# Kernel tuning notes

Measured on AMD Instinct MI355X. Metric: run time of the kernel, lower is better.

Reference implementation:

```python
import jax, jax.numpy as jnp
import numpy as np

SP_D, SP_H = 22, 11   # att_dim, number of vertical strips
EPS = 1e-5
ITER_N = 5            # Newton-Schulz iterations


def setup_inputs() -> dict:
    key = jax.random.key(0)
    ks = jax.random.split(key, 16)
    B, C, H, W = 64, 1024, 44, 16
    f = jnp.float32
    return {
        'x': jax.random.normal(ks[0], (B, C, H, W), dtype=f),
        'dr_w': jax.random.normal(ks[1], (SP_D, C), dtype=f) * 0.02,
        'dr_b': jax.random.normal(ks[2], (SP_D,), dtype=f) * 0.01,
        'bn1_g': 1.0 + 0.1 * jax.random.normal(ks[3], (SP_D,), dtype=f),
        'bn1_b': 0.1 * jax.random.normal(ks[4], (SP_D,), dtype=f),
        'bn1_m': 0.1 * jax.random.normal(ks[5], (SP_D,), dtype=f),
        'bn1_v': jax.random.uniform(ks[6], (SP_D,), dtype=f, minval=0.5, maxval=1.5),
        'rbn_g': 1.0 + 0.1 * jax.random.normal(ks[7], (SP_H,), dtype=f),
        'rbn_b': 0.1 * jax.random.normal(ks[8], (SP_H,), dtype=f),
        'rbn_m': 0.1 * jax.random.normal(ks[9], (SP_H,), dtype=f),
        'rbn_v': jax.random.uniform(ks[10], (SP_H,), dtype=f, minval=0.5, maxval=1.5),
        'rcw': jax.random.normal(ks[11], (SP_H, 4, SP_H), dtype=f) * 0.1,  # grouped conv: [group, out/group, kh]
        'rcb': jax.random.normal(ks[12], (SP_H, 4), dtype=f) * 0.01,
        'fcw': jax.random.normal(ks[13], (SP_H, 4 * SP_H), dtype=f) * 0.1,
        'fcb': jax.random.normal(ks[14], (SP_H,), dtype=f) * 0.01,
    }


def reference(x, dr_w, dr_b, bn1_g, bn1_b, bn1_m, bn1_v,
              rbn_g, rbn_b, rbn_m, rbn_v, rcw, rcb, fcw, fcb):
    B, C, H, W = x.shape
    # ReLU + 1x1 dimension-reduction conv + BN (eval mode, running stats)
    y = jax.nn.relu(x)
    y = jnp.einsum('bchw,dc->bdhw', y, dr_w) + dr_b[None, :, None, None]
    s1 = bn1_g / jnp.sqrt(bn1_v + EPS)
    y = (y - bn1_m[None, :, None, None]) * s1[None, :, None, None] + bn1_b[None, :, None, None]
    # adaptive avg pool to (11,1); H divisible by 11, pool over W entirely
    y = y.reshape(B, SP_D, SP_H, H // SP_H, W).mean(axis=(3, 4))   # [B,22,11]
    z = jnp.swapaxes(y, 1, 2)                                      # [B,11,22]: 11 strips, M=22 samples
    # MPNCOV covariance pooling: z @ I_hat @ z^T == centered outer product / M
    zc = z - z.mean(axis=2, keepdims=True)
    A = (zc @ jnp.swapaxes(zc, 1, 2)) / SP_D                       # [B,11,11]
    # Newton-Schulz matrix square root (MPNCOV SqrtmLayer, iterN=5)
    I3 = 3.0 * jnp.eye(SP_H, dtype=x.dtype)
    tr = jnp.trace(A, axis1=1, axis2=2)[:, None, None]             # normA = trace
    An = A / tr
    T = 0.5 * (I3 - An)
    Y, Z = An @ T, T
    for _ in range(ITER_N - 2):
        T = 0.5 * (I3 - Z @ Y)
        Y, Z = Y @ T, T @ Z
    S = 0.5 * (Y @ (I3 - Z @ Y)) * jnp.sqrt(tr)                    # [B,11,11]
    # row-wise BN (eval) over channel dim (rows of cov)
    rs = rbn_g / jnp.sqrt(rbn_v + EPS)
    v = (S - rbn_m[None, :, None]) * rs[None, :, None] + rbn_b[None, :, None]
    # grouped row conv: Conv2d(11, 44, kernel=(11,1), groups=11) -> [B,11,4]
    g = jax.nn.relu(jnp.einsum('bch,cjh->bcj', v, rcw) + rcb[None])
    # 1x1 fc 44 -> 11, sigmoid gate per strip
    a = jax.nn.sigmoid(g.reshape(B, 4 * SP_H) @ fcw.T + fcb[None])  # [B,11]
    # adaptive 'unpool' back to (H, W): exact repeat since H % 11 == 0
    att = jnp.repeat(a[:, None, :, None], H // SP_H, axis=2)        # [B,1,H,1]
    return jnp.broadcast_to(att, (B, 1, H, W))
```

## Files before the change

### kernel.cpp

```cpp
#include <hip/hip_runtime.h>
#include <math.h>

#define EPSV 1e-5f

__global__ __launch_bounds__(256) void pool_relu_kernel(
    const float* __restrict__ x, float* __restrict__ P)
{
    int t = blockIdx.x * blockDim.x + threadIdx.x;
    const float4 v = reinterpret_cast<const float4*>(x)[t];
    float s = fmaxf(v.x, 0.f) + fmaxf(v.y, 0.f) + fmaxf(v.z, 0.f) + fmaxf(v.w, 0.f);
    s += __shfl_xor(s, 1);
    s += __shfl_xor(s, 2);
    s += __shfl_xor(s, 4);
    s += __shfl_xor(s, 8);
    if ((threadIdx.x & 15) == 0) P[t >> 4] = s * (1.0f / 64.0f);
}

__global__ __launch_bounds__(256) void somm_tail_kernel(
    const float* __restrict__ P,
    const float* __restrict__ dr_w, const float* __restrict__ dr_b,
    const float* __restrict__ bn1_g, const float* __restrict__ bn1_b,
    const float* __restrict__ bn1_m, const float* __restrict__ bn1_v,
    const float* __restrict__ rbn_g, const float* __restrict__ rbn_b,
    const float* __restrict__ rbn_m, const float* __restrict__ rbn_v,
    const float* __restrict__ rcw, const float* __restrict__ rcb,
    const float* __restrict__ fcw, const float* __restrict__ fcb,
    float* __restrict__ out)
{
    const int b   = blockIdx.x;
    const int tid = threadIdx.x;

    __shared__ float Pl[11][1028];
    __shared__ float z[11][22];
    __shared__ float An[128], Tm[128], Ym[128], Zm[128], M1[128], Y2[128], Z2[128];
    __shared__ float zmean[11], trsh;
    __shared__ float gsh[44], ash[11];

    const float* Pb = P + b * (1024 * 11);
    for (int idx = tid; idx < 1024 * 11; idx += 256) {
        int c = idx / 11;
        int s = idx - c * 11;
        Pl[s][c] = Pb[idx];
    }
    __syncthreads();

    if (tid < 242) {
        int d = tid / 11, s = tid - d * 11;
        const float4* wrow = reinterpret_cast<const float4*>(dr_w + d * 1024);
        const float4* prow = reinterpret_cast<const float4*>(&Pl[s][0]);
        float acc = 0.f;
#pragma unroll 8
        for (int c4 = 0; c4 < 256; ++c4) {
            float4 w = wrow[c4];
            float4 p = prow[c4];
            acc += w.x * p.x + w.y * p.y + w.z * p.z + w.w * p.w;
        }
        float s1 = bn1_g[d] / sqrtf(bn1_v[d] + EPSV);
        z[s][d] = (acc + dr_b[d] - bn1_m[d]) * s1 + bn1_b[d];
    }
    __syncthreads();

    if (tid < 11) {
        float m = 0.f;
        for (int d2 = 0; d2 < 22; ++d2) m += z[tid][d2];
        zmean[tid] = m * (1.f / 22.f);
    }
    __syncthreads();

    const int i = tid / 11, j = tid - (tid / 11) * 11;

    if (tid < 121) {
        float mi = zmean[i], mj = zmean[j];
        float acc = 0.f;
        for (int d2 = 0; d2 < 22; ++d2)
            acc += (z[i][d2] - mi) * (z[j][d2] - mj);
        An[tid] = acc * (1.f / 22.f);
    }
    __syncthreads();
    if (tid == 0) {
        float tr = 0.f;
        for (int k = 0; k < 11; ++k) tr += An[k * 11 + k];
        trsh = tr;
    }
    __syncthreads();
    const float tr = trsh;

    if (tid < 121) {
        float an = An[tid] / tr;
        An[tid] = an;
        Tm[tid] = (i == j ? 1.5f : 0.f) - 0.5f * an;
    }
    __syncthreads();
    if (tid < 121) {
        float acc = 0.f;
        for (int k = 0; k < 11; ++k) acc += An[i * 11 + k] * Tm[k * 11 + j];
        Ym[tid] = acc;
        Zm[tid] = Tm[tid];
    }
    __syncthreads();

    for (int it = 0; it < 3; ++it) {
        if (tid < 121) {
            float acc = 0.f;
            for (int k = 0; k < 11; ++k) acc += Zm[i * 11 + k] * Ym[k * 11 + j];
            M1[tid] = acc;
        }
        __syncthreads();
        if (tid < 121) Tm[tid] = (i == j ? 1.5f : 0.f) - 0.5f * M1[tid];
        __syncthreads();
        if (tid < 121) {
            float accY = 0.f, accZ = 0.f;
            for (int k = 0; k < 11; ++k) {
                accY += Ym[i * 11 + k] * Tm[k * 11 + j];
                accZ += Tm[i * 11 + k] * Zm[k * 11 + j];
            }
            Y2[tid] = accY;
            Z2[tid] = accZ;
        }
        __syncthreads();
        if (tid < 121) { Ym[tid] = Y2[tid]; Zm[tid] = Z2[tid]; }
        __syncthreads();
    }

    if (tid < 121) {
        float acc = 0.f;
        for (int k = 0; k < 11; ++k) acc += Zm[i * 11 + k] * Ym[k * 11 + j];
        M1[tid] = (i == j ? 3.f : 0.f) - acc;
    }
    __syncthreads();
    if (tid < 121) {
        float acc = 0.f;
        for (int k = 0; k < 11; ++k) acc += Ym[i * 11 + k] * M1[k * 11 + j];
        float S  = 0.5f * acc * sqrtf(tr);
        float rs = rbn_g[i] / sqrtf(rbn_v[i] + EPSV);
        Y2[tid]  = (S - rbn_m[i]) * rs + rbn_b[i];
    }
    __syncthreads();

    if (tid < 44) {
        int c = tid >> 2;
        float acc = rcb[tid];
        for (int h = 0; h < 11; ++h) acc += Y2[c * 11 + h] * rcw[tid * 11 + h];
        gsh[tid] = fmaxf(acc, 0.f);
    }
    __syncthreads();

    if (tid < 11) {
        float acc = fcb[tid];
        for (int k = 0; k < 44; ++k) acc += gsh[k] * fcw[tid * 44 + k];
        ash[tid] = 1.f / (1.f + expf(-acc));
    }
    __syncthreads();

    for (int idx = tid; idx < 704; idx += 256) {
        out[b * 704 + idx] = ash[idx >> 6];
    }
}

extern "C" void kernel_launch(void* const* d_in, const int* in_sizes, int n_in,
                              void* d_out, int out_size, void* d_ws, size_t ws_size,
                              hipStream_t stream) {
    const float* x     = (const float*)d_in[0];
    const float* dr_w  = (const float*)d_in[1];
    const float* dr_b  = (const float*)d_in[2];
    const float* bn1_g = (const float*)d_in[3];
    const float* bn1_b = (const float*)d_in[4];
    const float* bn1_m = (const float*)d_in[5];
    const float* bn1_v = (const float*)d_in[6];
    const float* rbn_g = (const float*)d_in[7];
    const float* rbn_b = (const float*)d_in[8];
    const float* rbn_m = (const float*)d_in[9];
    const float* rbn_v = (const float*)d_in[10];
    const float* rcw   = (const float*)d_in[11];
    const float* rcb   = (const float*)d_in[12];
    const float* fcw   = (const float*)d_in[13];
    const float* fcb   = (const float*)d_in[14];
    float* out = (float*)d_out;
    float* P   = (float*)d_ws;

    pool_relu_kernel<<<45056, 256, 0, stream>>>(x, P);
    somm_tail_kernel<<<64, 256, 0, stream>>>(P, dr_w, dr_b, bn1_g, bn1_b, bn1_m,
                                             bn1_v, rbn_g, rbn_b, rbn_m, rbn_v,
                                             rcw, rcb, fcw, fcb, out);
}
```

Baseline: 293.4 us.

## Fuse ReLU pooling with 1x1 reduction into per-channel-group partial sums

Merges the ReLU+pool pass with the 22x1024 channel reduction. Each block now handles 32 channels of one batch item and writes 242 partial dot products. The tail kernel only sums 32 partials per output, so it no longer serially streams a 45KB pooled tensor and runs a 1024-long dot product in just 64 blocks. The cost is fewer, longer-running blocks in the bandwidth-bound first kernel (22 loads per thread) and a small extra partial-sum buffer.

After: 292.0 us. Within noise of the previous version (-0.5%).

```diff
diff --git a/kernel.cpp b/kernel.cpp
--- a/kernel.cpp
+++ b/kernel.cpp
@@ -3,22 +3,50 @@
 
 #define EPSV 1e-5f
 
-__global__ __launch_bounds__(256) void pool_relu_kernel(
-    const float* __restrict__ x, float* __restrict__ P)
+__global__ __launch_bounds__(256) void fused_pool_mm_kernel(
+    const float* __restrict__ x, const float* __restrict__ dr_w,
+    float* __restrict__ zpart)
 {
-    int t = blockIdx.x * blockDim.x + threadIdx.x;
-    const float4 v = reinterpret_cast<const float4*>(x)[t];
-    float s = fmaxf(v.x, 0.f) + fmaxf(v.y, 0.f) + fmaxf(v.z, 0.f) + fmaxf(v.w, 0.f);
-    s += __shfl_xor(s, 1);
-    s += __shfl_xor(s, 2);
-    s += __shfl_xor(s, 4);
-    s += __shfl_xor(s, 8);
-    if ((threadIdx.x & 15) == 0) P[t >> 4] = s * (1.0f / 64.0f);
+    __shared__ float Pl[352];
+    const int t  = threadIdx.x;
+    const int b  = blockIdx.x >> 5;
+    const int cg = blockIdx.x & 31;
+    const int c0 = cg * 32;
+
+    const float4* x4 = reinterpret_cast<const float4*>(x)
+                     + (size_t)(b * 1024 + c0) * 176;
+#pragma unroll
+    for (int k = 0; k < 22; ++k) {
+        float4 v = x4[k * 256 + t];
+        float s = fmaxf(v.x, 0.f) + fmaxf(v.y, 0.f)
+                + fmaxf(v.z, 0.f) + fmaxf(v.w, 0.f);
+        s += __shfl_xor(s, 1);
+        s += __shfl_xor(s, 2);
+        s += __shfl_xor(s, 4);
+        s += __shfl_xor(s, 8);
+        if ((t & 15) == 0) Pl[k * 16 + (t >> 4)] = s * (1.f / 64.f);
+    }
+    __syncthreads();
+
+    if (t < 242) {
+        const int d = t / 11, sIdx = t - d * 11;
+        const float4* wr = reinterpret_cast<const float4*>(dr_w + d * 1024 + c0);
+        float acc = 0.f;
+#pragma unroll
+        for (int q = 0; q < 8; ++q) {
+            float4 w = wr[q];
+            acc += w.x * Pl[(4 * q + 0) * 11 + sIdx]
+                 + w.y * Pl[(4 * q + 1) * 11 + sIdx]
+                 + w.z * Pl[(4 * q + 2) * 11 + sIdx]
+                 + w.w * Pl[(4 * q + 3) * 11 + sIdx];
+        }
+        zpart[blockIdx.x * 242 + t] = acc;
+    }
 }
 
 __global__ __launch_bounds__(256) void somm_tail_kernel(
-    const float* __restrict__ P,
-    const float* __restrict__ dr_w, const float* __restrict__ dr_b,
+    const float* __restrict__ zpart,
+    const float* __restrict__ dr_b,
     const float* __restrict__ bn1_g, const float* __restrict__ bn1_b,
     const float* __restrict__ bn1_m, const float* __restrict__ bn1_v,
     const float* __restrict__ rbn_g, const float* __restrict__ rbn_b,
@@ -30,33 +58,19 @@
     const int b   = blockIdx.x;
     const int tid = threadIdx.x;
 
-    __shared__ float Pl[11][1028];
     __shared__ float z[11][22];
     __shared__ float An[128], Tm[128], Ym[128], Zm[128], M1[128], Y2[128], Z2[128];
     __shared__ float zmean[11], trsh;
     __shared__ float gsh[44], ash[11];
 
-    const float* Pb = P + b * (1024 * 11);
-    for (int idx = tid; idx < 1024 * 11; idx += 256) {
-        int c = idx / 11;
-        int s = idx - c * 11;
-        Pl[s][c] = Pb[idx];
-    }
-    __syncthreads();
-
     if (tid < 242) {
-        int d = tid / 11, s = tid - d * 11;
-        const float4* wrow = reinterpret_cast<const float4*>(dr_w + d * 1024);
-        const float4* prow = reinterpret_cast<const float4*>(&Pl[s][0]);
+        const int d = tid / 11, sIdx = tid - d * 11;
         float acc = 0.f;
-#pragma unroll 8
-        for (int c4 = 0; c4 < 256; ++c4) {
-            float4 w = wrow[c4];
-            float4 p = prow[c4];
-            acc += w.x * p.x + w.y * p.y + w.z * p.z + w.w * p.w;
-        }
+#pragma unroll
+        for (int cg = 0; cg < 32; ++cg)
+            acc += zpart[(b * 32 + cg) * 242 + tid];
         float s1 = bn1_g[d] / sqrtf(bn1_v[d] + EPSV);
-        z[s][d] = (acc + dr_b[d] - bn1_m[d]) * s1 + bn1_b[d];
+        z[sIdx][d] = (acc + dr_b[d] - bn1_m[d]) * s1 + bn1_b[d];
     }
     __syncthreads();
 
@@ -175,11 +189,11 @@
     const float* rcb   = (const float*)d_in[12];
     const float* fcw   = (const float*)d_in[13];
     const float* fcb   = (const float*)d_in[14];
-    float* out = (float*)d_out;
-    float* P   = (float*)d_ws;
+    float* out   = (float*)d_out;
+    float* zpart = (float*)d_ws;
 
-    pool_relu_kernel<<<45056, 256, 0, stream>>>(x, P);
-    somm_tail_kernel<<<64, 256, 0, stream>>>(P, dr_w, dr_b, bn1_g, bn1_b, bn1_m,
+    fused_pool_mm_kernel<<<64 * 32, 256, 0, stream>>>(x, dr_w, zpart);
+    somm_tail_kernel<<<64, 256, 0, stream>>>(zpart, dr_b, bn1_g, bn1_b, bn1_m,
                                              bn1_v, rbn_g, rbn_b, rbn_m, rbn_v,
                                              rcw, rcb, fcw, fcb, out);
 }
```
